# Kernel optimization log

Measured on AMD Instinct MI355X. Metric: run time of the kernel, lower is better.

The kernel has to match this reference:

```python
import jax, jax.numpy as jnp
import numpy as np

N_NODES = 50000
N_EDGES = 800000
D_IN = 64
D_OUT = 64


def setup_inputs() -> dict:
    key = jax.random.key(0)
    k1, k2, k3, k4 = jax.random.split(key, 4)
    x = jax.random.normal(k1, (N_NODES, D_IN), dtype=jnp.float32)
    edge_index = jax.random.randint(k2, (2, N_EDGES), 0, N_NODES, dtype=jnp.int64)
    scale = np.sqrt(1.0 / D_IN).astype(np.float32)
    W_msg = jax.random.normal(k3, (D_OUT, D_IN), dtype=jnp.float32) * scale
    W_self = jax.random.normal(k4, (D_OUT, D_IN), dtype=jnp.float32) * scale
    b_msg = jnp.zeros((D_OUT,), dtype=jnp.float32)
    b_self = jnp.zeros((D_OUT,), dtype=jnp.float32)
    return {"x": x, "edge_index": edge_index, "W_msg": W_msg, "b_msg": b_msg,
            "W_self": W_self, "b_self": b_self}


def reference(x, edge_index, W_msg, b_msg, W_self, b_self):
    row, col = edge_index[0], edge_index[1]
    n = x.shape[0]
    # message projection on all source nodes, then gather per edge
    msgs_src = x @ W_msg.T + b_msg            # [N, D_OUT]
    per_edge = msgs_src[row]                  # [E, D_OUT] gather
    # scatter-mean into destination nodes
    summed = jax.ops.segment_sum(per_edge, col, num_segments=n)          # [N, D_OUT]
    counts = jax.ops.segment_sum(jnp.ones_like(col, dtype=x.dtype), col,
                                 num_segments=n)                         # [N]
    agg = summed / jnp.maximum(counts, 1.0)[:, None]
    self_out = x @ W_self.T + b_self
    return self_out + agg
```

## Files before the change

kernel.cpp:

```cpp
#include <hip/hip_runtime.h>

constexpr int N_NODES = 50000;
constexpr int N_EDGES = 800000;
constexpr int D = 64;
constexpr int NB = (N_NODES + 63) / 64;
constexpr int BUCKET_CAP = 1536;
constexpr unsigned ZERO_ROW = 50000u;

typedef __attribute__((ext_vector_type(8))) short short8;
typedef __attribute__((ext_vector_type(4))) float f32x4;

static __device__ inline unsigned short f2bf(float f) {
    unsigned u = __float_as_uint(f);
    unsigned r = (u + 0x7FFFu + ((u >> 16) & 1u)) >> 16;
    return (unsigned short)r;
}
static __device__ inline unsigned pack2(float lo, float hi) {
    return (unsigned)f2bf(lo) | ((unsigned)f2bf(hi) << 16);
}
static __device__ inline float bf2f(unsigned short b) {
    return __uint_as_float((unsigned)b << 16);
}

constexpr int BIN_BLOCKS = 256;
constexpr int EDGES_PER_BIN_BLOCK = (N_EDGES + BIN_BLOCKS - 1) / BIN_BLOCKS;

__global__ __launch_bounds__(512) void k_bin_place(
    const float* __restrict__ x, unsigned short* __restrict__ xb,
    const float* __restrict__ W_msg, const float* __restrict__ W_self,
    unsigned short* __restrict__ B_packed,
    const int* __restrict__ edge_index,
    unsigned* __restrict__ g_cursor, unsigned* __restrict__ bucket_data)
{
    __shared__ unsigned ent_sh[EDGES_PER_BIN_BLOCK];
    __shared__ unsigned lcount[NB];
    __shared__ unsigned lbase[NB];

    int tid = threadIdx.x;

    for (int b = tid; b < NB; b += 512) lcount[b] = 0u;

    int gid = blockIdx.x * 512 + tid;
    for (int t = gid; t < N_NODES * D / 4; t += BIN_BLOCKS * 512) {
        float4 v = ((const float4*)x)[t];
        uint2 p;
        p.x = pack2(v.x, v.y);
        p.y = pack2(v.z, v.w);
        ((uint2*)xb)[t] = p;
    }
    if (blockIdx.x == 0) {
        for (int idx = tid; idx < 64 * 128; idx += 512) {
            int n = idx >> 7;
            int k = idx & 127;
            float v = (k < 64) ? W_self[n * 64 + k] : W_msg[n * 64 + (k - 64)];
            B_packed[idx] = f2bf(v);
        }
    } else if (blockIdx.x == 1) {
        if (tid < 8)
            *(uint4*)&xb[ZERO_ROW * D + tid * 8] = make_uint4(0u, 0u, 0u, 0u);
    }

    int e0 = blockIdx.x * EDGES_PER_BIN_BLOCK;
    int e1 = min(e0 + EDGES_PER_BIN_BLOCK, N_EDGES);
    int ne = e1 - e0;
    __syncthreads();

    for (int e = e0 + tid; e < e1; e += 512) {
        int dst = edge_index[N_EDGES + e];
        int src = edge_index[e];
        ent_sh[e - e0] = ((unsigned)src << 16) | (unsigned)dst;
        atomicAdd(&lcount[dst >> 6], 1u);
    }
    __syncthreads();

    for (int b = tid; b < NB; b += 512) {
        unsigned c = lcount[b];
        lbase[b] = c ? ((unsigned)b * BUCKET_CAP + atomicAdd(&g_cursor[b], c)) : 0u;
    }
    __syncthreads();
    for (int b = tid; b < NB; b += 512) lcount[b] = 0u;
    __syncthreads();

    for (int i = tid; i < ne; i += 512) {
        unsigned ent = ent_sh[i];
        unsigned dst = ent & 0xFFFFu;
        unsigned b   = dst >> 6;
        unsigned off = atomicAdd(&lcount[b], 1u);
        bucket_data[lbase[b] + off] = (ent >> 16) | ((dst & 63u) << 16);
    }
}

constexpr int A_STRIDE = 136;

__global__ __launch_bounds__(512) void k_fused(
    const unsigned short* __restrict__ x_bf16,
    const unsigned short* __restrict__ B_packed,
    const float* __restrict__ b_msg, const float* __restrict__ b_self,
    const unsigned* __restrict__ cursor,
    const unsigned* __restrict__ bucket_data,
    float* __restrict__ out)
{
    __shared__ __align__(16) unsigned short A_sh[64 * A_STRIDE];
    __shared__ __align__(16) unsigned short B_sh[64 * A_STRIDE];
    __shared__ unsigned short sorted_sh[BUCKET_CAP];
    __shared__ unsigned cnt_sh[64];
    __shared__ unsigned poff_sh[64];
    __shared__ unsigned woff_sh[64];

    int tid  = threadIdx.x;
    int w    = tid >> 6;
    int lane = tid & 63;
    int r0   = blockIdx.x * 64;

    unsigned start = (unsigned)blockIdx.x * BUCKET_CAP;
    unsigned end   = start + cursor[blockIdx.x];

    unsigned i0 = start + (unsigned)tid;
    unsigned i1 = i0 + 512u;
    unsigned i2 = i1 + 512u;
    unsigned ent0 = 0u, ent1 = 0u, ent2 = 0u;
    bool v0 = i0 < end, v1 = i1 < end, v2 = i2 < end;
    if (v0) ent0 = bucket_data[i0];
    if (v1) ent1 = bucket_data[i1];
    if (v2) ent2 = bucket_data[i2];

    if (tid < 64) cnt_sh[tid] = 0u;
    for (int idx = tid; idx < 64 * 8; idx += 512) {
        int row = idx >> 3;
        int c   = idx & 7;
        int g   = r0 + row;
        uint4 v = make_uint4(0u, 0u, 0u, 0u);
        if (g < N_NODES) v = *(const uint4*)&x_bf16[g * D + c * 8];
        *(uint4*)&A_sh[row * A_STRIDE + c * 8] = v;
    }
    for (int idx = tid; idx < 64 * 16; idx += 512) {
        int n = idx >> 4;
        int c = idx & 15;
        uint4 v = *(const uint4*)&B_packed[n * 128 + c * 8];
        *(uint4*)&B_sh[n * A_STRIDE + c * 8] = v;
    }
    for (int i = tid; i < BUCKET_CAP; i += 512)
        sorted_sh[i] = (unsigned short)ZERO_ROW;

    if (v0) atomicAdd(&cnt_sh[ent0 >> 16], 1u);
    if (v1) atomicAdd(&cnt_sh[ent1 >> 16], 1u);
    if (v2) atomicAdd(&cnt_sh[ent2 >> 16], 1u);
    __syncthreads();

    if (tid < 64) {
        unsigned c  = cnt_sh[tid];
        unsigned pc = (c + 7u) & ~7u;
        unsigned xsum = pc;
        #pragma unroll
        for (int s = 1; s < 64; s <<= 1) {
            unsigned v = (unsigned)__shfl_up((int)xsum, s);
            if (lane >= s) xsum += v;
        }
        poff_sh[tid] = xsum - pc;
        woff_sh[tid] = xsum - pc;
    }
    __syncthreads();

    if (v0) {
        unsigned slot = atomicAdd(&woff_sh[ent0 >> 16], 1u);
        sorted_sh[slot] = (unsigned short)(ent0 & 0xFFFFu);
    }
    if (v1) {
        unsigned slot = atomicAdd(&woff_sh[ent1 >> 16], 1u);
        sorted_sh[slot] = (unsigned short)(ent1 & 0xFFFFu);
    }
    if (v2) {
        unsigned slot = atomicAdd(&woff_sh[ent2 >> 16], 1u);
        sorted_sh[slot] = (unsigned short)(ent2 & 0xFFFFu);
    }
    __syncthreads();

    int Q = lane >> 4;
    int f = lane & 15;

    #pragma unroll
    for (int pass = 0; pass < 2; ++pass) {
        int lrow = w * 8 + pass * 4 + Q;
        unsigned s0 = poff_sh[lrow];
        unsigned dc = cnt_sh[lrow];
        unsigned pc = (dc + 7u) & ~7u;

        float a0 = 0.f, a1 = 0.f, a2 = 0.f, a3 = 0.f;
        for (unsigned j = 0; j < pc; j += 8u) {
            ushort4 rv[8];
            #pragma unroll
            for (int u = 0; u < 8; ++u) {
                unsigned src = (unsigned)sorted_sh[s0 + j + u];
                rv[u] = *(const ushort4*)&x_bf16[(src << 6) + 4u * (unsigned)f];
            }
            #pragma unroll
            for (int u = 0; u < 8; ++u) {
                a0 += bf2f(rv[u].x); a1 += bf2f(rv[u].y);
                a2 += bf2f(rv[u].z); a3 += bf2f(rv[u].w);
            }
        }
        float inv = dc ? 1.0f / (float)dc : 0.0f;
        uint2 p;
        p.x = pack2(a0 * inv, a1 * inv);
        p.y = pack2(a2 * inv, a3 * inv);
        *(uint2*)&A_sh[lrow * A_STRIDE + 64 + 4 * f] = p;
    }
    __syncthreads();

    int wm   = w & 3;
    int ng   = (w >> 2) * 2;
    int quad = lane >> 4;
    int l15  = lane & 15;

    f32x4 accr[2] = {{0.f,0.f,0.f,0.f},{0.f,0.f,0.f,0.f}};

    #pragma unroll
    for (int k0 = 0; k0 < 128; k0 += 32) {
        short8 a = *(const short8*)&A_sh[(16 * wm + l15) * A_STRIDE + k0 + quad * 8];
        #pragma unroll
        for (int t = 0; t < 2; ++t) {
            short8 b = *(const short8*)&B_sh[(16 * (ng + t) + l15) * A_STRIDE + k0 + quad * 8];
            accr[t] = __builtin_amdgcn_mfma_f32_16x16x32_bf16(a, b, accr[t], 0, 0, 0);
        }
    }

    #pragma unroll
    for (int t = 0; t < 2; ++t) {
        int col = (ng + t) * 16 + l15;
        float bs = b_self[col];
        float bm = b_msg[col];
        #pragma unroll
        for (int r = 0; r < 4; ++r) {
            int lrow = 16 * wm + quad * 4 + r;
            int grow = r0 + lrow;
            if (grow < N_NODES) {
                float vv = accr[t][r] + bs + (cnt_sh[lrow] > 0u ? bm : 0.0f);
                out[grow * D + col] = vv;
            }
        }
    }
}

extern "C" void kernel_launch(void* const* d_in, const int* in_sizes, int n_in,
                              void* d_out, int out_size, void* d_ws, size_t ws_size,
                              hipStream_t stream) {
    const float* x      = (const float*)d_in[0];
    const int*   edges  = (const int*)  d_in[1];
    const float* W_msg  = (const float*)d_in[2];
    const float* b_msg  = (const float*)d_in[3];
    const float* W_self = (const float*)d_in[4];
    const float* b_self = (const float*)d_in[5];
    float*       out    = (float*)d_out;

    char* ws = (char*)d_ws;
    unsigned*       cursor      = (unsigned*)(ws + 0);
    unsigned short* B_packed    = (unsigned short*)(ws + 4096);
    unsigned*       bucket_data = (unsigned*)(ws + 20480);
    unsigned short* x_bf16      = (unsigned short*)(ws + 20480 + (size_t)NB * BUCKET_CAP * 4);

    hipMemsetAsync(cursor, 0, NB * sizeof(unsigned), stream);

    k_bin_place<<<BIN_BLOCKS, 512, 0, stream>>>(x, x_bf16, W_msg, W_self,
                                                B_packed, edges, cursor, bucket_data);
    k_fused<<<NB, 512, 0, stream>>>(x_bf16, B_packed, b_msg, b_self,
                                    cursor, bucket_data, out);
}
```

Before: 114.1 us.

## Interleave two row gathers per wave, vectorize index reads, double bin blocks

The neighbor gather now processes both destination rows of a thread in one loop, issuing 16 independent bf16 row loads per iteration instead of 8. The goal is more memory-level parallelism to hide gather latency. Source indices are read from shared memory as 16-byte vectors. Out-of-range slots point at a zero row. Separately, the binning kernel doubles its block count and uses a second counter array, which removes one reset and one barrier. The trade-off is extra registers, plus wasted loads when the two rows have very different degrees.

```diff
diff --git a/kernel.cpp b/kernel.cpp
--- a/kernel.cpp
+++ b/kernel.cpp
@@ -22,7 +22,7 @@
     return __uint_as_float((unsigned)b << 16);
 }
 
-constexpr int BIN_BLOCKS = 256;
+constexpr int BIN_BLOCKS = 512;
 constexpr int EDGES_PER_BIN_BLOCK = (N_EDGES + BIN_BLOCKS - 1) / BIN_BLOCKS;
 
 __global__ __launch_bounds__(512) void k_bin_place(
@@ -34,11 +34,12 @@
 {
     __shared__ unsigned ent_sh[EDGES_PER_BIN_BLOCK];
     __shared__ unsigned lcount[NB];
+    __shared__ unsigned lcur[NB];
     __shared__ unsigned lbase[NB];
 
     int tid = threadIdx.x;
 
-    for (int b = tid; b < NB; b += 512) lcount[b] = 0u;
+    for (int b = tid; b < NB; b += 512) { lcount[b] = 0u; lcur[b] = 0u; }
 
     int gid = blockIdx.x * 512 + tid;
     for (int t = gid; t < N_NODES * D / 4; t += BIN_BLOCKS * 512) {
@@ -78,14 +79,12 @@
         lbase[b] = c ? ((unsigned)b * BUCKET_CAP + atomicAdd(&g_cursor[b], c)) : 0u;
     }
     __syncthreads();
-    for (int b = tid; b < NB; b += 512) lcount[b] = 0u;
-    __syncthreads();
 
     for (int i = tid; i < ne; i += 512) {
         unsigned ent = ent_sh[i];
         unsigned dst = ent & 0xFFFFu;
         unsigned b   = dst >> 6;
-        unsigned off = atomicAdd(&lcount[b], 1u);
+        unsigned off = atomicAdd(&lcur[b], 1u);
         bucket_data[lbase[b] + off] = (ent >> 16) | ((dst & 63u) << 16);
     }
 }
@@ -102,7 +101,7 @@
 {
     __shared__ __align__(16) unsigned short A_sh[64 * A_STRIDE];
     __shared__ __align__(16) unsigned short B_sh[64 * A_STRIDE];
-    __shared__ unsigned short sorted_sh[BUCKET_CAP];
+    __shared__ __align__(16) unsigned short sorted_sh[BUCKET_CAP];
     __shared__ unsigned cnt_sh[64];
     __shared__ unsigned poff_sh[64];
     __shared__ unsigned woff_sh[64];
@@ -178,32 +177,50 @@
     int Q = lane >> 4;
     int f = lane & 15;
 
-    #pragma unroll
-    for (int pass = 0; pass < 2; ++pass) {
-        int lrow = w * 8 + pass * 4 + Q;
-        unsigned s0 = poff_sh[lrow];
-        unsigned dc = cnt_sh[lrow];
-        unsigned pc = (dc + 7u) & ~7u;
-
-        float a0 = 0.f, a1 = 0.f, a2 = 0.f, a3 = 0.f;
-        for (unsigned j = 0; j < pc; j += 8u) {
-            ushort4 rv[8];
-            #pragma unroll
-            for (int u = 0; u < 8; ++u) {
-                unsigned src = (unsigned)sorted_sh[s0 + j + u];
-                rv[u] = *(const ushort4*)&x_bf16[(src << 6) + 4u * (unsigned)f];
-            }
-            #pragma unroll
-            for (int u = 0; u < 8; ++u) {
-                a0 += bf2f(rv[u].x); a1 += bf2f(rv[u].y);
-                a2 += bf2f(rv[u].z); a3 += bf2f(rv[u].w);
-            }
-        }
-        float inv = dc ? 1.0f / (float)dc : 0.0f;
+    int lrowA = w * 8 + Q;
+    int lrowB = w * 8 + 4 + Q;
+    unsigned sA = poff_sh[lrowA], dA = cnt_sh[lrowA], pA = (dA + 7u) & ~7u;
+    unsigned sB = poff_sh[lrowB], dB = cnt_sh[lrowB], pB = (dB + 7u) & ~7u;
+    unsigned pMax = pA > pB ? pA : pB;
+
+    float aA0 = 0.f, aA1 = 0.f, aA2 = 0.f, aA3 = 0.f;
+    float aB0 = 0.f, aB1 = 0.f, aB2 = 0.f, aB3 = 0.f;
+
+    for (unsigned j = 0; j < pMax; j += 8u) {
+        ushort4 eAlo = make_ushort4(ZERO_ROW,ZERO_ROW,ZERO_ROW,ZERO_ROW), eAhi = eAlo;
+        ushort4 eBlo = eAlo, eBhi = eAlo;
+        if (j < pA) { const uint4 t = *(const uint4*)&sorted_sh[sA + j];
+                      eAlo = *(const ushort4*)&t.x; eAhi = *(const ushort4*)&t.z; }
+        if (j < pB) { const uint4 t = *(const uint4*)&sorted_sh[sB + j];
+                      eBlo = *(const ushort4*)&t.x; eBhi = *(const ushort4*)&t.z; }
+        unsigned srcs[16] = {
+            eAlo.x, eAlo.y, eAlo.z, eAlo.w, eAhi.x, eAhi.y, eAhi.z, eAhi.w,
+            eBlo.x, eBlo.y, eBlo.z, eBlo.w, eBhi.x, eBhi.y, eBhi.z, eBhi.w };
+        ushort4 rv[16];
+        #pragma unroll
+        for (int u = 0; u < 16; ++u)
+            rv[u] = *(const ushort4*)&x_bf16[((unsigned)srcs[u] << 6) + 4u * (unsigned)f];
+        #pragma unroll
+        for (int u = 0; u < 8; ++u) {
+            aA0 += bf2f(rv[u].x); aA1 += bf2f(rv[u].y);
+            aA2 += bf2f(rv[u].z); aA3 += bf2f(rv[u].w);
+        }
+        #pragma unroll
+        for (int u = 8; u < 16; ++u) {
+            aB0 += bf2f(rv[u].x); aB1 += bf2f(rv[u].y);
+            aB2 += bf2f(rv[u].z); aB3 += bf2f(rv[u].w);
+        }
+    }
+    {
+        float invA = dA ? 1.0f / (float)dA : 0.0f;
         uint2 p;
-        p.x = pack2(a0 * inv, a1 * inv);
-        p.y = pack2(a2 * inv, a3 * inv);
-        *(uint2*)&A_sh[lrow * A_STRIDE + 64 + 4 * f] = p;
+        p.x = pack2(aA0 * invA, aA1 * invA);
+        p.y = pack2(aA2 * invA, aA3 * invA);
+        *(uint2*)&A_sh[lrowA * A_STRIDE + 64 + 4 * f] = p;
+        float invB = dB ? 1.0f / (float)dB : 0.0f;
+        p.x = pack2(aB0 * invB, aB1 * invB);
+        p.y = pack2(aB2 * invB, aB3 * invB);
+        *(uint2*)&A_sh[lrowB * A_STRIDE + 64 + 4 * f] = p;
     }
     __syncthreads();
 
```

New measurement: 119.1 us. 4.4% more time.
